# Kernel optimization log

Hardware: AMD Instinct MI355X
Metric: run time of the kernel (lower is better)

## Reference

```python
import jax, jax.numpy as jnp
import numpy as np

B, T, D_OBS, D_ACT, H = 1024, 1024, 32, 4, 64


def setup_inputs() -> dict:
    key = jax.random.key(0)
    ks = jax.random.split(key, 8)
    s = 0.1
    obs = jax.random.normal(ks[0], (B, T, D_OBS), dtype=jnp.float32)
    action = jax.random.normal(ks[1], (B, T, D_ACT), dtype=jnp.float32)
    # GRUCell params (torch layout): weight_ih [3H, Din], weight_hh [3H, H]
    W_ih = jax.random.normal(ks[2], (3 * H, D_OBS + D_ACT), dtype=jnp.float32) * s
    W_hh = jax.random.normal(ks[3], (3 * H, H), dtype=jnp.float32) * s
    b_ih = jax.random.normal(ks[4], (3 * H,), dtype=jnp.float32) * s
    b_hh = jax.random.normal(ks[5], (3 * H,), dtype=jnp.float32) * s
    # reward head: Linear(H, 1)
    W_r = jax.random.normal(ks[6], (1, H), dtype=jnp.float32) * s
    b_r = jax.random.normal(ks[7], (1,), dtype=jnp.float32) * s
    return {"obs": obs, "action": action, "W_ih": W_ih, "b_ih": b_ih,
            "W_hh": W_hh, "b_hh": b_hh, "W_r": W_r, "b_r": b_r}


def reference(obs, action, W_ih, b_ih, W_hh, b_hh, W_r, b_r):
    # x_t = cat(obs_t, action_t); GRUCell recurrence; reward = Linear(h_t)
    x = jnp.concatenate([obs, action], axis=-1)              # [B, T, Din]
    # Precompute input-to-hidden gates for all timesteps (batched GEMM)
    gi = jnp.einsum('btd,gd->btg', x, W_ih) + b_ih           # [B, T, 3H]
    gi_t = jnp.swapaxes(gi, 0, 1)                            # [T, B, 3H]

    def step(h, gi_step):
        gh = h @ W_hh.T + b_hh                               # [B, 3H]
        ghr, ghz, ghn = jnp.split(gh, 3, axis=-1)
        gir, giz, gin = jnp.split(gi_step, 3, axis=-1)
        r = jax.nn.sigmoid(gir + ghr)
        z = jax.nn.sigmoid(giz + ghz)
        n = jnp.tanh(gin + r * ghn)
        h_new = (1.0 - z) * n + z * h
        reward = h_new @ W_r.T + b_r                         # [B, 1]
        return h_new, reward

    h0 = jnp.zeros((obs.shape[0], H), dtype=obs.dtype)
    h_final, rewards = jax.lax.scan(step, h0, gi_t)          # rewards: [T, B, 1]
    return h_final, jnp.swapaxes(rewards, 0, 1)              # h: [B, H], reward: [B, T, 1]
```

## Files before the change

kernel.cpp:

```cpp
#include <hip/hip_runtime.h>


#define BB 1024
#define TT 1024
#define DOBS 32
#define DACT 4
#define HH 64

typedef __attribute__((ext_vector_type(8))) short short8;
typedef __attribute__((ext_vector_type(4))) float f32x4;

#define MFMA(A, B, C) __builtin_amdgcn_mfma_f32_16x16x32_bf16((A), (B), (C), 0, 0, 0)

static __device__ __forceinline__ unsigned short f2bf(float f) {
    unsigned u = __float_as_uint(f);
    u += 0x7fffu + ((u >> 16) & 1u);
    return (unsigned short)(u >> 16);
}
static __device__ __forceinline__ float frcp(float x) { return __builtin_amdgcn_rcpf(x); }
static __device__ __forceinline__ unsigned cvt_pk(float lo, float hi) {
    unsigned r;
    asm("v_cvt_pk_bf16_f32 %0, %1, %2" : "=v"(r) : "v"(lo), "v"(hi));
    return r;
}

#define L2E 1.442695040888963f

__global__ __launch_bounds__(256)
void pack_x(const float* __restrict__ obs, const float* __restrict__ act,
            unsigned short* __restrict__ xext)
{
    const size_t r = (size_t)blockIdx.x * 256 + threadIdx.x;
    const float* o = obs + r * DOBS;
    unsigned short* d = xext + r * 40;
    short8 v[5];
#pragma unroll
    for (int j = 0; j < 4; ++j) {
        float4 a = ((const float4*)o)[2 * j];
        float4 b = ((const float4*)o)[2 * j + 1];
        short8 t;
        t[0]=f2bf(a.x); t[1]=f2bf(a.y); t[2]=f2bf(a.z); t[3]=f2bf(a.w);
        t[4]=f2bf(b.x); t[5]=f2bf(b.y); t[6]=f2bf(b.z); t[7]=f2bf(b.w);
        v[j] = t;
    }
    {
        float4 a = *(const float4*)(act + r * DACT);
        short8 t;
        t[0]=f2bf(a.x); t[1]=f2bf(a.y); t[2]=f2bf(a.z); t[3]=f2bf(a.w);
        t[4]=(short)0x3f80; t[5]=0; t[6]=0; t[7]=0;
        v[4] = t;
    }
#pragma unroll
    for (int j = 0; j < 5; ++j) ((short8*)d)[j] = v[j];
}

#define LOADX(XO, XA, T)                                                       \
  {                                                                            \
    if (PACKED) {                                                              \
      XO = *(const short8*)(px + (size_t)(T) * 40 + 8 * q);                    \
      XA = (q == 0) ? *(const short8*)(px + (size_t)(T) * 40 + 32) : zero8;    \
    } else {                                                                   \
      const int tc_ = (T) < TT ? (T) : TT - 1;                                 \
      const float* op_ = po + (size_t)tc_ * DOBS + 8 * q;                      \
      float4 a_ = *(const float4*)op_, b_ = *(const float4*)(op_ + 4);         \
      short8 f_;                                                               \
      f_[0]=f2bf(a_.x); f_[1]=f2bf(a_.y); f_[2]=f2bf(a_.z); f_[3]=f2bf(a_.w);  \
      f_[4]=f2bf(b_.x); f_[5]=f2bf(b_.y); f_[6]=f2bf(b_.z); f_[7]=f2bf(b_.w);  \
      XO = f_;                                                                 \
      if (q == 0) {                                                            \
        float4 av_ = *(const float4*)(pa + (size_t)tc_ * DACT);                \
        short8 g_;                                                             \
        g_[0]=f2bf(av_.x); g_[1]=f2bf(av_.y); g_[2]=f2bf(av_.z);               \
        g_[3]=f2bf(av_.w); g_[4]=(short)0x3f80; g_[5]=0; g_[6]=0; g_[7]=0;     \
        XA = g_;                                                               \
      } else XA = zero8;                                                       \
    }                                                                          \
  }

#define HEAVY(PH, T, IT)                                                       \
  {                                                                            \
    __builtin_amdgcn_s_setprio(1);                                             \
    short8 Ah0 = *(const short8*)((const char*)hbuf[PH] + rdaddr0);            \
    short8 Ah1 = *(const short8*)((const char*)hbuf[PH] + rdaddr1);            \
    f32x4 hp = *(const f32x4*)((const char*)hf32[PH] + f32addr);               \
    f32x4 Cr  = MFMA(AH[0][1], Ah1, MFMA(AH[0][0], Ah0, cgr));                 \
    f32x4 Cz  = MFMA(AH[1][1], Ah1, MFMA(AH[1][0], Ah0, cgz));                 \
    f32x4 Cnh = MFMA(AH[2][1], Ah1, MFMA(AH[2][0], Ah0, bhn4));                \
    f32x4 Crw = zf;                                                            \
    const bool dorw_ = (w == ((IT) & 3));                                      \
    if (dorw_) Crw = MFMA(AR[1], Ah1, MFMA(AR[0], Ah0, zf));                   \
    _Pragma("unroll")                                                          \
    for (int reg = 0; reg < 4; ++reg) {                                        \
      float rr   = frcp(1.0f + __builtin_amdgcn_exp2f(Cr[reg]));               \
      float zz   = frcp(1.0f + __builtin_amdgcn_exp2f(Cz[reg]));               \
      float E    = __builtin_amdgcn_exp2f(__builtin_fmaf(rr, Cnh[reg], cgn[reg])); \
      float nn   = __builtin_fmaf(-2.0f, frcp(E + 1.0f), 1.0f);                \
      hold[reg]  = __builtin_fmaf(zz, hp[reg] - nn, nn);                       \
    }                                                                          \
    unsigned pk0 = cvt_pk(hold[0], hold[1]);                                   \
    unsigned pk1 = cvt_pk(hold[2], hold[3]);                                   \
    *(uint2*)((char*)hbuf[PH ^ 1] + wraddr) = make_uint2(pk0, pk1);            \
    *(f32x4*)((char*)hf32[PH ^ 1] + f32addr) = hold;                           \
    if (dorw_ && q == 0 && (T) > 0)                                            \
      rew[(size_t)(bid * 16 + c) * TT + (T) - 1] = Crw[0] + brr;               \
    asm volatile("s_waitcnt lgkmcnt(0)" ::: "memory");                         \
    __builtin_amdgcn_s_setprio(0);                                             \
  }

#define LIGHT(T2)                                                              \
  {                                                                            \
    cgr = MFMA(AX[0][1], xa, MFMA(AX[0][0], xo, zf));                          \
    cgz = MFMA(AX[1][1], xa, MFMA(AX[1][0], xo, zf));                          \
    cgn = MFMA(AX[2][1], xa, MFMA(AX[2][0], xo, zf));                          \
    LOADX(xo, xa, (T2) + 2)                                                    \
  }

template<bool PACKED>
__global__ __launch_bounds__(512, 1)
void gru_fused(const unsigned short* __restrict__ xext,
               const float* __restrict__ obs, const float* __restrict__ act,
               const float* __restrict__ W_ih, const float* __restrict__ b_ih,
               const float* __restrict__ W_hh, const float* __restrict__ b_hh,
               const float* __restrict__ W_r, const float* __restrict__ b_r,
               float* __restrict__ out)
{
    const int tid = threadIdx.x;
    const int set = tid >> 8;
    const int w = (tid >> 6) & 3;
    const int l = tid & 63, c = l & 15, q = l >> 4;
    const int bid = blockIdx.x;
    const int u0 = 16 * w + 4 * q;

    __shared__ __align__(16) unsigned short hbuf[2][16 * 64];
    __shared__ __align__(16) float          hf32[2][16 * 64];

    short8 AX[3][2], AH[3][2];
#pragma unroll
    for (int m = 0; m < 3; ++m) {
        const float sc = (m == 2) ? (2.0f * L2E) : (-L2E);
        const int j = w + 4 * m;
        const int g = 16 * j + c;
        {
            const float* wp = W_ih + (size_t)g * 36 + 8 * q;
            float4 a = *(const float4*)wp, b = *(const float4*)(wp + 4);
            short8 f;
            f[0]=f2bf(a.x*sc); f[1]=f2bf(a.y*sc); f[2]=f2bf(a.z*sc); f[3]=f2bf(a.w*sc);
            f[4]=f2bf(b.x*sc); f[5]=f2bf(b.y*sc); f[6]=f2bf(b.z*sc); f[7]=f2bf(b.w*sc);
            AX[m][0] = f;
        }
        {
            short8 f;
#pragma unroll
            for (int i = 0; i < 8; ++i) {
                int k = 32 + 8 * q + i;
                float v = 0.f;
                if (k < 36)       v = W_ih[(size_t)g * 36 + k];
                else if (k == 36) v = b_ih[g] + (g < 128 ? b_hh[g] : 0.f);
                f[i] = f2bf(v * sc);
            }
            AX[m][1] = f;
        }
#pragma unroll
        for (int kk = 0; kk < 2; ++kk) {
            const float* wp = W_hh + (size_t)g * HH + 32 * kk + 8 * q;
            float4 a = *(const float4*)wp, b = *(const float4*)(wp + 4);
            short8 f;
            f[0]=f2bf(a.x*sc); f[1]=f2bf(a.y*sc); f[2]=f2bf(a.z*sc); f[3]=f2bf(a.w*sc);
            f[4]=f2bf(b.x*sc); f[5]=f2bf(b.y*sc); f[6]=f2bf(b.z*sc); f[7]=f2bf(b.w*sc);
            AH[m][kk] = f;
        }
    }
    short8 AR[2];
#pragma unroll
    for (int kk = 0; kk < 2; ++kk) {
        short8 f;
#pragma unroll
        for (int i = 0; i < 8; ++i) {
            int k = 32 * kk + 8 * q + i;
            f[i] = (c == 0) ? (short)f2bf(W_r[k]) : (short)0;
        }
        AR[kk] = f;
    }

    f32x4 bhn4;
#pragma unroll
    for (int reg = 0; reg < 4; ++reg) bhn4[reg] = b_hh[128 + u0 + reg] * (2.0f * L2E);
    const float brr = b_r[0];

    const int swz = c & 7;
    const int wraddr  = c * 128 + ((((u0 >> 3)) ^ swz) << 4) + (u0 & 7) * 2;
    const int rdaddr0 = c * 128 + ((q ^ swz) << 4);
    const int rdaddr1 = c * 128 + (((4 + q) ^ swz) << 4);
    const int f32addr = c * 256 + (((4 * w + q) ^ swz) << 4);

    const size_t row = (size_t)(bid * 16 + c) * TT;
    const unsigned short* px = xext + row * 40;
    const float* po = obs + row * DOBS;
    const float* pa = act + row * DACT;

    const short8 zero8 = {0, 0, 0, 0, 0, 0, 0, 0};
    const f32x4 zf = {0.f, 0.f, 0.f, 0.f};

    ((uint2*)hbuf)[tid] = make_uint2(0u, 0u);
    ((f32x4*)hf32)[tid] = zf;
    short8 xo, xa;
    f32x4 cgr = zf, cgz = zf, cgn = zf;
    if (set == 0) {
        LOADX(xo, xa, 0)
        cgr = MFMA(AX[0][1], xa, MFMA(AX[0][0], xo, zf));
        cgz = MFMA(AX[1][1], xa, MFMA(AX[1][0], xo, zf));
        cgn = MFMA(AX[2][1], xa, MFMA(AX[2][0], xo, zf));
        LOADX(xo, xa, 2)
    } else {
        LOADX(xo, xa, 1)
    }
    f32x4 hold = zf;
    asm volatile("s_waitcnt lgkmcnt(0)" ::: "memory");
    __builtin_amdgcn_s_barrier();
    asm volatile("" ::: "memory");

    float* rew = out + (size_t)BB * HH;

#pragma unroll 1
    for (int it = 0; it < TT / 2; ++it) {
        const int Ta = 2 * it, Tb = 2 * it + 1;
        if (set == 0) { HEAVY(0, Ta, it) } else { LIGHT(Tb) }
        __builtin_amdgcn_s_barrier();
        asm volatile("" ::: "memory");
        if (set == 1) { HEAVY(1, Tb, it) } else { LIGHT(Ta + 2) }
        __builtin_amdgcn_s_barrier();
        asm volatile("" ::: "memory");
    }

    if (set == 1) {
        if (w == 3) {
            short8 Ah0 = *(const short8*)((const char*)hbuf[0] + rdaddr0);
            short8 Ah1 = *(const short8*)((const char*)hbuf[0] + rdaddr1);
            f32x4 Crw = MFMA(AR[0], Ah0, zf);
            Crw = MFMA(AR[1], Ah1, Crw);
            if (q == 0)
                rew[(size_t)(bid * 16 + c) * TT + TT - 1] = Crw[0] + brr;
        }
        *(float4*)(out + (size_t)(bid * 16 + c) * HH + u0) =
            make_float4(hold[0], hold[1], hold[2], hold[3]);
    }
}

extern "C" void kernel_launch(void* const* d_in, const int* in_sizes, int n_in,
                              void* d_out, int out_size, void* d_ws, size_t ws_size,
                              hipStream_t stream)
{
    const float* obs    = (const float*)d_in[0];
    const float* action = (const float*)d_in[1];
    const float* W_ih   = (const float*)d_in[2];
    const float* b_ih   = (const float*)d_in[3];
    const float* W_hh   = (const float*)d_in[4];
    const float* b_hh   = (const float*)d_in[5];
    const float* W_r    = (const float*)d_in[6];
    const float* b_r    = (const float*)d_in[7];
    float* out          = (float*)d_out;

    const size_t xext_bytes = ((size_t)BB * TT + 8) * 40 * sizeof(unsigned short);
    if (ws_size >= xext_bytes) {
        unsigned short* xext = (unsigned short*)d_ws;
        pack_x<<<dim3((BB * TT) / 256), dim3(256), 0, stream>>>(obs, action, xext);
        gru_fused<true><<<dim3(BB / 16), dim3(512), 0, stream>>>(
            xext, obs, action, W_ih, b_ih, W_hh, b_hh, W_r, b_r, out);
    } else {
        gru_fused<false><<<dim3(BB / 16), dim3(512), 0, stream>>>(
            nullptr, obs, action, W_ih, b_ih, W_hh, b_hh, W_r, b_r, out);
    }
}
```

Baseline: 398.7 us.

## Process two independent 16-row batch tiles per block to interleave recurrence chains

Each block now handles 32 batch rows as two independent 16-row tiles (X and Y), with separate LDS hidden-state buffers and duplicated MFMA/gate work. The grid shrinks from 64 to 32 blocks. The aim is to give the instruction scheduler two independent dependency chains to interleave, hiding MFMA and transcendental latency in the serial time loop. The trade-off is that only half as many CUs are used, on a GPU with far more CUs than blocks. The unpacked fallback path is replaced by a simple per-batch wave kernel.

```diff
diff --git a/kernel.cpp b/kernel.cpp
--- a/kernel.cpp
+++ b/kernel.cpp
@@ -54,71 +54,70 @@
     for (int j = 0; j < 5; ++j) ((short8*)d)[j] = v[j];
 }
 
-#define LOADX(XO, XA, T)                                                       \
+#define LOADX(PX, XO, XA, T)                                                   \
   {                                                                            \
-    if (PACKED) {                                                              \
-      XO = *(const short8*)(px + (size_t)(T) * 40 + 8 * q);                    \
-      XA = (q == 0) ? *(const short8*)(px + (size_t)(T) * 40 + 32) : zero8;    \
-    } else {                                                                   \
-      const int tc_ = (T) < TT ? (T) : TT - 1;                                 \
-      const float* op_ = po + (size_t)tc_ * DOBS + 8 * q;                      \
-      float4 a_ = *(const float4*)op_, b_ = *(const float4*)(op_ + 4);         \
-      short8 f_;                                                               \
-      f_[0]=f2bf(a_.x); f_[1]=f2bf(a_.y); f_[2]=f2bf(a_.z); f_[3]=f2bf(a_.w);  \
-      f_[4]=f2bf(b_.x); f_[5]=f2bf(b_.y); f_[6]=f2bf(b_.z); f_[7]=f2bf(b_.w);  \
-      XO = f_;                                                                 \
-      if (q == 0) {                                                            \
-        float4 av_ = *(const float4*)(pa + (size_t)tc_ * DACT);                \
-        short8 g_;                                                             \
-        g_[0]=f2bf(av_.x); g_[1]=f2bf(av_.y); g_[2]=f2bf(av_.z);               \
-        g_[3]=f2bf(av_.w); g_[4]=(short)0x3f80; g_[5]=0; g_[6]=0; g_[7]=0;     \
-        XA = g_;                                                               \
-      } else XA = zero8;                                                       \
+    XO = *(const short8*)((PX) + (size_t)(T) * 40 + 8 * q);                    \
+    XA = (q == 0) ? *(const short8*)((PX) + (size_t)(T) * 40 + 32) : zero8;    \
+  }
+
+#define GATES(CRF, CZF, CNHF, CNIF, HP, HOLD, HB, F32, PH)                     \
+    _Pragma("unroll")                                                          \
+    for (int reg = 0; reg < 4; ++reg) {                                        \
+      float rr   = frcp(1.0f + __builtin_amdgcn_exp2f(CRF[reg]));              \
+      float zz   = frcp(1.0f + __builtin_amdgcn_exp2f(CZF[reg]));              \
+      float E    = __builtin_amdgcn_exp2f(__builtin_fmaf(rr, CNHF[reg], CNIF[reg])); \
+      float nn   = __builtin_fmaf(-2.0f, frcp(E + 1.0f), 1.0f);                \
+      HOLD[reg]  = __builtin_fmaf(zz, HP[reg] - nn, nn);                       \
     }                                                                          \
-  }
+    *(uint2*)((char*)HB[PH ^ 1] + wraddr) =                                    \
+        make_uint2(cvt_pk(HOLD[0], HOLD[1]), cvt_pk(HOLD[2], HOLD[3]));        \
+    *(f32x4*)((char*)F32[PH ^ 1] + f32addr) = HOLD;
 
 #define HEAVY(PH, T, IT)                                                       \
   {                                                                            \
     __builtin_amdgcn_s_setprio(1);                                             \
-    short8 Ah0 = *(const short8*)((const char*)hbuf[PH] + rdaddr0);            \
-    short8 Ah1 = *(const short8*)((const char*)hbuf[PH] + rdaddr1);            \
-    f32x4 hp = *(const f32x4*)((const char*)hf32[PH] + f32addr);               \
-    f32x4 Cr  = MFMA(AH[0][1], Ah1, MFMA(AH[0][0], Ah0, cgr));                 \
-    f32x4 Cz  = MFMA(AH[1][1], Ah1, MFMA(AH[1][0], Ah0, cgz));                 \
-    f32x4 Cnh = MFMA(AH[2][1], Ah1, MFMA(AH[2][0], Ah0, bhn4));                \
-    f32x4 Crw = zf;                                                            \
+    short8 Ax0 = *(const short8*)((const char*)hbX[PH] + rdaddr0);             \
+    short8 Ax1 = *(const short8*)((const char*)hbX[PH] + rdaddr1);             \
+    short8 Ay0 = *(const short8*)((const char*)hbY[PH] + rdaddr0);             \
+    short8 Ay1 = *(const short8*)((const char*)hbY[PH] + rdaddr1);             \
+    f32x4 hpX = *(const f32x4*)((const char*)hfX[PH] + f32addr);               \
+    f32x4 hpY = *(const f32x4*)((const char*)hfY[PH] + f32addr);               \
+    f32x4 CrX  = MFMA(AH[0][1], Ax1, MFMA(AH[0][0], Ax0, cgrX));               \
+    f32x4 CrY  = MFMA(AH[0][1], Ay1, MFMA(AH[0][0], Ay0, cgrY));               \
+    f32x4 CzX  = MFMA(AH[1][1], Ax1, MFMA(AH[1][0], Ax0, cgzX));               \
+    f32x4 CzY  = MFMA(AH[1][1], Ay1, MFMA(AH[1][0], Ay0, cgzY));               \
+    f32x4 CnhX = MFMA(AH[2][1], Ax1, MFMA(AH[2][0], Ax0, bhn4));               \
+    f32x4 CnhY = MFMA(AH[2][1], Ay1, MFMA(AH[2][0], Ay0, bhn4));               \
+    f32x4 CrwX = zf, CrwY = zf;                                                \
     const bool dorw_ = (w == ((IT) & 3));                                      \
-    if (dorw_) Crw = MFMA(AR[1], Ah1, MFMA(AR[0], Ah0, zf));                   \
-    _Pragma("unroll")                                                          \
-    for (int reg = 0; reg < 4; ++reg) {                                        \
-      float rr   = frcp(1.0f + __builtin_amdgcn_exp2f(Cr[reg]));               \
-      float zz   = frcp(1.0f + __builtin_amdgcn_exp2f(Cz[reg]));               \
-      float E    = __builtin_amdgcn_exp2f(__builtin_fmaf(rr, Cnh[reg], cgn[reg])); \
-      float nn   = __builtin_fmaf(-2.0f, frcp(E + 1.0f), 1.0f);                \
-      hold[reg]  = __builtin_fmaf(zz, hp[reg] - nn, nn);                       \
+    if (dorw_) {                                                               \
+      CrwX = MFMA(AR[1], Ax1, MFMA(AR[0], Ax0, zf));                           \
+      CrwY = MFMA(AR[1], Ay1, MFMA(AR[0], Ay0, zf));                           \
     }                                                                          \
-    unsigned pk0 = cvt_pk(hold[0], hold[1]);                                   \
-    unsigned pk1 = cvt_pk(hold[2], hold[3]);                                   \
-    *(uint2*)((char*)hbuf[PH ^ 1] + wraddr) = make_uint2(pk0, pk1);            \
-    *(f32x4*)((char*)hf32[PH ^ 1] + f32addr) = hold;                           \
-    if (dorw_ && q == 0 && (T) > 0)                                            \
-      rew[(size_t)(bid * 16 + c) * TT + (T) - 1] = Crw[0] + brr;               \
+    GATES(CrX, CzX, CnhX, cgnX, hpX, holdX, hbX, hfX, PH)                      \
+    GATES(CrY, CzY, CnhY, cgnY, hpY, holdY, hbY, hfY, PH)                      \
+    if (dorw_ && q == 0 && (T) > 0) {                                          \
+      rew[(size_t)(bid * 32 + c) * TT + (T) - 1]      = CrwX[0] + brr;         \
+      rew[(size_t)(bid * 32 + 16 + c) * TT + (T) - 1] = CrwY[0] + brr;         \
+    }                                                                          \
     asm volatile("s_waitcnt lgkmcnt(0)" ::: "memory");                         \
     __builtin_amdgcn_s_setprio(0);                                             \
   }
 
 #define LIGHT(T2)                                                              \
   {                                                                            \
-    cgr = MFMA(AX[0][1], xa, MFMA(AX[0][0], xo, zf));                          \
-    cgz = MFMA(AX[1][1], xa, MFMA(AX[1][0], xo, zf));                          \
-    cgn = MFMA(AX[2][1], xa, MFMA(AX[2][0], xo, zf));                          \
-    LOADX(xo, xa, (T2) + 2)                                                    \
+    cgrX = MFMA(AX[0][1], xaX, MFMA(AX[0][0], xoX, zf));                       \
+    cgrY = MFMA(AX[0][1], xaY, MFMA(AX[0][0], xoY, zf));                       \
+    cgzX = MFMA(AX[1][1], xaX, MFMA(AX[1][0], xoX, zf));                       \
+    cgzY = MFMA(AX[1][1], xaY, MFMA(AX[1][0], xoY, zf));                       \
+    cgnX = MFMA(AX[2][1], xaX, MFMA(AX[2][0], xoX, zf));                       \
+    cgnY = MFMA(AX[2][1], xaY, MFMA(AX[2][0], xoY, zf));                       \
+    LOADX(pxX, xoX, xaX, (T2) + 2)                                             \
+    LOADX(pxY, xoY, xaY, (T2) + 2)                                             \
   }
 
-template<bool PACKED>
 __global__ __launch_bounds__(512, 1)
 void gru_fused(const unsigned short* __restrict__ xext,
-               const float* __restrict__ obs, const float* __restrict__ act,
                const float* __restrict__ W_ih, const float* __restrict__ b_ih,
                const float* __restrict__ W_hh, const float* __restrict__ b_hh,
                const float* __restrict__ W_r, const float* __restrict__ b_r,
@@ -131,8 +130,8 @@
     const int bid = blockIdx.x;
     const int u0 = 16 * w + 4 * q;
 
-    __shared__ __align__(16) unsigned short hbuf[2][16 * 64];
-    __shared__ __align__(16) float          hf32[2][16 * 64];
+    __shared__ __align__(16) unsigned short hbX[2][16 * 64], hbY[2][16 * 64];
+    __shared__ __align__(16) float          hfX[2][16 * 64], hfY[2][16 * 64];
 
     short8 AX[3][2], AH[3][2];
 #pragma unroll
@@ -193,28 +192,34 @@
     const int rdaddr1 = c * 128 + (((4 + q) ^ swz) << 4);
     const int f32addr = c * 256 + (((4 * w + q) ^ swz) << 4);
 
-    const size_t row = (size_t)(bid * 16 + c) * TT;
-    const unsigned short* px = xext + row * 40;
-    const float* po = obs + row * DOBS;
-    const float* pa = act + row * DACT;
+    const unsigned short* pxX = xext + ((size_t)(bid * 32 + c) * TT) * 40;
+    const unsigned short* pxY = xext + ((size_t)(bid * 32 + 16 + c) * TT) * 40;
 
     const short8 zero8 = {0, 0, 0, 0, 0, 0, 0, 0};
     const f32x4 zf = {0.f, 0.f, 0.f, 0.f};
 
-    ((uint2*)hbuf)[tid] = make_uint2(0u, 0u);
-    ((f32x4*)hf32)[tid] = zf;
-    short8 xo, xa;
-    f32x4 cgr = zf, cgz = zf, cgn = zf;
+    ((uint2*)hbX)[tid] = make_uint2(0u, 0u);
+    ((uint2*)hbY)[tid] = make_uint2(0u, 0u);
+    ((f32x4*)hfX)[tid] = zf;
+    ((f32x4*)hfY)[tid] = zf;
+    short8 xoX, xaX, xoY, xaY;
+    f32x4 cgrX = zf, cgzX = zf, cgnX = zf, cgrY = zf, cgzY = zf, cgnY = zf;
     if (set == 0) {
-        LOADX(xo, xa, 0)
-        cgr = MFMA(AX[0][1], xa, MFMA(AX[0][0], xo, zf));
-        cgz = MFMA(AX[1][1], xa, MFMA(AX[1][0], xo, zf));
-        cgn = MFMA(AX[2][1], xa, MFMA(AX[2][0], xo, zf));
-        LOADX(xo, xa, 2)
+        LOADX(pxX, xoX, xaX, 0)
+        LOADX(pxY, xoY, xaY, 0)
+        cgrX = MFMA(AX[0][1], xaX, MFMA(AX[0][0], xoX, zf));
+        cgrY = MFMA(AX[0][1], xaY, MFMA(AX[0][0], xoY, zf));
+        cgzX = MFMA(AX[1][1], xaX, MFMA(AX[1][0], xoX, zf));
+        cgzY = MFMA(AX[1][1], xaY, MFMA(AX[1][0], xoY, zf));
+        cgnX = MFMA(AX[2][1], xaX, MFMA(AX[2][0], xoX, zf));
+        cgnY = MFMA(AX[2][1], xaY, MFMA(AX[2][0], xoY, zf));
+        LOADX(pxX, xoX, xaX, 2)
+        LOADX(pxY, xoY, xaY, 2)
     } else {
-        LOADX(xo, xa, 1)
-    }
-    f32x4 hold = zf;
+        LOADX(pxX, xoX, xaX, 1)
+        LOADX(pxY, xoY, xaY, 1)
+    }
+    f32x4 holdX = zf, holdY = zf;
     asm volatile("s_waitcnt lgkmcnt(0)" ::: "memory");
     __builtin_amdgcn_s_barrier();
     asm volatile("" ::: "memory");
@@ -234,16 +239,74 @@
 
     if (set == 1) {
         if (w == 3) {
-            short8 Ah0 = *(const short8*)((const char*)hbuf[0] + rdaddr0);
-            short8 Ah1 = *(const short8*)((const char*)hbuf[0] + rdaddr1);
-            f32x4 Crw = MFMA(AR[0], Ah0, zf);
-            Crw = MFMA(AR[1], Ah1, Crw);
-            if (q == 0)
-                rew[(size_t)(bid * 16 + c) * TT + TT - 1] = Crw[0] + brr;
-        }
-        *(float4*)(out + (size_t)(bid * 16 + c) * HH + u0) =
-            make_float4(hold[0], hold[1], hold[2], hold[3]);
-    }
+            short8 Ax0 = *(const short8*)((const char*)hbX[0] + rdaddr0);
+            short8 Ax1 = *(const short8*)((const char*)hbX[0] + rdaddr1);
+            short8 Ay0 = *(const short8*)((const char*)hbY[0] + rdaddr0);
+            short8 Ay1 = *(const short8*)((const char*)hbY[0] + rdaddr1);
+            f32x4 CrwX = MFMA(AR[1], Ax1, MFMA(AR[0], Ax0, zf));
+            f32x4 CrwY = MFMA(AR[1], Ay1, MFMA(AR[0], Ay0, zf));
+            if (q == 0) {
+                rew[(size_t)(bid * 32 + c) * TT + TT - 1]      = CrwX[0] + brr;
+                rew[(size_t)(bid * 32 + 16 + c) * TT + TT - 1] = CrwY[0] + brr;
+            }
+        }
+        *(float4*)(out + (size_t)(bid * 32 + c) * HH + u0) =
+            make_float4(holdX[0], holdX[1], holdX[2], holdX[3]);
+        *(float4*)(out + (size_t)(bid * 32 + 16 + c) * HH + u0) =
+            make_float4(holdY[0], holdY[1], holdY[2], holdY[3]);
+    }
+}
+
+__global__ __launch_bounds__(64, 1)
+void gru_wave_fb(const float* __restrict__ obs, const float* __restrict__ action,
+                 const float* __restrict__ W_ih, const float* __restrict__ b_ih,
+                 const float* __restrict__ W_hh, const float* __restrict__ b_hh,
+                 const float* __restrict__ W_r, const float* __restrict__ b_r,
+                 float* __restrict__ out)
+{
+    const int b = blockIdx.x, j = threadIdx.x;
+    float wir[36], wiz[36], win[36];
+#pragma unroll
+    for (int d = 0; d < 36; ++d) {
+        wir[d] = W_ih[(size_t)(0 * HH + j) * 36 + d];
+        wiz[d] = W_ih[(size_t)(1 * HH + j) * 36 + d];
+        win[d] = W_ih[(size_t)(2 * HH + j) * 36 + d];
+    }
+    float whr[HH], whz[HH], whn[HH];
+#pragma unroll
+    for (int k = 0; k < HH; ++k) {
+        whr[k] = W_hh[(size_t)(0 * HH + j) * HH + k];
+        whz[k] = W_hh[(size_t)(1 * HH + j) * HH + k];
+        whn[k] = W_hh[(size_t)(2 * HH + j) * HH + k];
+    }
+    const float bir = b_ih[j], biz = b_ih[HH + j], bin = b_ih[2 * HH + j];
+    const float bhr = b_hh[j], bhz = b_hh[HH + j], bhn = b_hh[2 * HH + j];
+    const float wr = W_r[j], br = b_r[0];
+    float h = 0.f;
+    float* rew = out + (size_t)BB * HH;
+    for (int t = 0; t < TT; ++t) {
+        float x[36];
+#pragma unroll
+        for (int d = 0; d < DOBS; ++d) x[d] = obs[((size_t)b * TT + t) * DOBS + d];
+#pragma unroll
+        for (int d = 0; d < DACT; ++d) x[32 + d] = action[((size_t)b * TT + t) * DACT + d];
+        float gr = bir + bhr, gz = biz + bhz, gn = bin, an = bhn;
+#pragma unroll
+        for (int d = 0; d < 36; ++d) { gr += wir[d]*x[d]; gz += wiz[d]*x[d]; gn += win[d]*x[d]; }
+#pragma unroll
+        for (int k = 0; k < HH; ++k) {
+            float hk = __int_as_float(__builtin_amdgcn_readlane(__float_as_int(h), k));
+            gr += whr[k]*hk; gz += whz[k]*hk; an += whn[k]*hk;
+        }
+        float r = frcp(1.f + __expf(-gr)), z = frcp(1.f + __expf(-gz));
+        float n = 1.f - 2.f*frcp(__expf(2.f*(gn + r*an)) + 1.f);
+        h = n + z*(h - n);
+        float pr = h * wr;
+#pragma unroll
+        for (int m = 1; m < 64; m <<= 1) pr += __shfl_xor(pr, m, 64);
+        if (j == 0) rew[(size_t)b * TT + t] = pr + br;
+    }
+    out[(size_t)b * HH + j] = h;
 }
 
 extern "C" void kernel_launch(void* const* d_in, const int* in_sizes, int n_in,
@@ -264,10 +327,10 @@
     if (ws_size >= xext_bytes) {
         unsigned short* xext = (unsigned short*)d_ws;
         pack_x<<<dim3((BB * TT) / 256), dim3(256), 0, stream>>>(obs, action, xext);
-        gru_fused<true><<<dim3(BB / 16), dim3(512), 0, stream>>>(
-            xext, obs, action, W_ih, b_ih, W_hh, b_hh, W_r, b_r, out);
+        gru_fused<<<dim3(BB / 32), dim3(512), 0, stream>>>(
+            xext, W_ih, b_ih, W_hh, b_hh, W_r, b_r, out);
     } else {
-        gru_fused<false><<<dim3(BB / 16), dim3(512), 0, stream>>>(
-            nullptr, obs, action, W_ih, b_ih, W_hh, b_hh, W_r, b_r, out);
-    }
-}
+        gru_wave_fb<<<dim3(BB), dim3(64), 0, stream>>>(
+            obs, action, W_ih, b_ih, W_hh, b_hh, W_r, b_r, out);
+    }
+}
```

Result: slower. 626.8 us (+57.2%).

## Drop bf16 pack prekernel; load fp32 inputs directly with deeper prefetch

Applied to the files above, without the earlier changes.

Removes the separate pack_x kernel that converted obs/action to a bf16 workspace, so the recurrent kernel reads fp32 inputs straight from global memory. Raw loads are issued two steps ahead into registers and converted with packed cvt instructions just before use, hiding the extra load latency. This cuts a full extra pass over the input tensors and a kernel launch, at the cost of reading fp32 (larger) data inside the latency-critical loop and holding more registers.

```diff
diff --git a/kernel.cpp b/kernel.cpp
--- a/kernel.cpp
+++ b/kernel.cpp
@@ -26,55 +26,25 @@
 
 #define L2E 1.442695040888963f
 
-__global__ __launch_bounds__(256)
-void pack_x(const float* __restrict__ obs, const float* __restrict__ act,
-            unsigned short* __restrict__ xext)
-{
-    const size_t r = (size_t)blockIdx.x * 256 + threadIdx.x;
-    const float* o = obs + r * DOBS;
-    unsigned short* d = xext + r * 40;
-    short8 v[5];
-#pragma unroll
-    for (int j = 0; j < 4; ++j) {
-        float4 a = ((const float4*)o)[2 * j];
-        float4 b = ((const float4*)o)[2 * j + 1];
-        short8 t;
-        t[0]=f2bf(a.x); t[1]=f2bf(a.y); t[2]=f2bf(a.z); t[3]=f2bf(a.w);
-        t[4]=f2bf(b.x); t[5]=f2bf(b.y); t[6]=f2bf(b.z); t[7]=f2bf(b.w);
-        v[j] = t;
-    }
-    {
-        float4 a = *(const float4*)(act + r * DACT);
-        short8 t;
-        t[0]=f2bf(a.x); t[1]=f2bf(a.y); t[2]=f2bf(a.z); t[3]=f2bf(a.w);
-        t[4]=(short)0x3f80; t[5]=0; t[6]=0; t[7]=0;
-        v[4] = t;
-    }
-#pragma unroll
-    for (int j = 0; j < 5; ++j) ((short8*)d)[j] = v[j];
-}
-
-#define LOADX(XO, XA, T)                                                       \
-  {                                                                            \
-    if (PACKED) {                                                              \
-      XO = *(const short8*)(px + (size_t)(T) * 40 + 8 * q);                    \
-      XA = (q == 0) ? *(const short8*)(px + (size_t)(T) * 40 + 32) : zero8;    \
-    } else {                                                                   \
-      const int tc_ = (T) < TT ? (T) : TT - 1;                                 \
-      const float* op_ = po + (size_t)tc_ * DOBS + 8 * q;                      \
-      float4 a_ = *(const float4*)op_, b_ = *(const float4*)(op_ + 4);         \
-      short8 f_;                                                               \
-      f_[0]=f2bf(a_.x); f_[1]=f2bf(a_.y); f_[2]=f2bf(a_.z); f_[3]=f2bf(a_.w);  \
-      f_[4]=f2bf(b_.x); f_[5]=f2bf(b_.y); f_[6]=f2bf(b_.z); f_[7]=f2bf(b_.w);  \
-      XO = f_;                                                                 \
-      if (q == 0) {                                                            \
-        float4 av_ = *(const float4*)(pa + (size_t)tc_ * DACT);                \
-        short8 g_;                                                             \
-        g_[0]=f2bf(av_.x); g_[1]=f2bf(av_.y); g_[2]=f2bf(av_.z);               \
-        g_[3]=f2bf(av_.w); g_[4]=(short)0x3f80; g_[5]=0; g_[6]=0; g_[7]=0;     \
-        XA = g_;                                                               \
-      } else XA = zero8;                                                       \
-    }                                                                          \
+#define LOADR(T2)                                                              \
+  {                                                                            \
+    const int tc_ = (T2) < TT ? (T2) : TT - 1;                                 \
+    const float* op_ = po + (size_t)tc_ * DOBS + 8 * q;                        \
+    rawA = *(const float4*)op_;                                                \
+    rawB = *(const float4*)(op_ + 4);                                          \
+    if (q == 0) rawC = *(const float4*)(pa + (size_t)tc_ * DACT);              \
+  }
+
+#define CVTX(XO, XA)                                                           \
+  {                                                                            \
+    uint4 u_ = make_uint4(cvt_pk(rawA.x, rawA.y), cvt_pk(rawA.z, rawA.w),      \
+                          cvt_pk(rawB.x, rawB.y), cvt_pk(rawB.z, rawB.w));     \
+    XO = *(short8*)&u_;                                                        \
+    if (q == 0) {                                                              \
+      uint4 v_ = make_uint4(cvt_pk(rawC.x, rawC.y), cvt_pk(rawC.z, rawC.w),    \
+                            0x3f80u, 0u);                \
+      XA = *(short8*)&v_;                                                      \
+    } else XA = zero8;                                                         \
   }
 
 #define HEAVY(PH, T, IT)                                                       \
@@ -112,13 +82,12 @@
     cgr = MFMA(AX[0][1], xa, MFMA(AX[0][0], xo, zf));                          \
     cgz = MFMA(AX[1][1], xa, MFMA(AX[1][0], xo, zf));                          \
     cgn = MFMA(AX[2][1], xa, MFMA(AX[2][0], xo, zf));                          \
-    LOADX(xo, xa, (T2) + 2)                                                    \
-  }
-
-template<bool PACKED>
+    CVTX(xo, xa)                                                               \
+    LOADR((T2) + 4)                                                            \
+  }
+
 __global__ __launch_bounds__(512, 1)
-void gru_fused(const unsigned short* __restrict__ xext,
-               const float* __restrict__ obs, const float* __restrict__ act,
+void gru_fused(const float* __restrict__ obs, const float* __restrict__ act,
                const float* __restrict__ W_ih, const float* __restrict__ b_ih,
                const float* __restrict__ W_hh, const float* __restrict__ b_hh,
                const float* __restrict__ W_r, const float* __restrict__ b_r,
@@ -194,7 +163,6 @@
     const int f32addr = c * 256 + (((4 * w + q) ^ swz) << 4);
 
     const size_t row = (size_t)(bid * 16 + c) * TT;
-    const unsigned short* px = xext + row * 40;
     const float* po = obs + row * DOBS;
     const float* pa = act + row * DACT;
 
@@ -203,16 +171,19 @@
 
     ((uint2*)hbuf)[tid] = make_uint2(0u, 0u);
     ((f32x4*)hf32)[tid] = zf;
+    float4 rawA = make_float4(0,0,0,0), rawB = rawA, rawC = rawA;
     short8 xo, xa;
     f32x4 cgr = zf, cgz = zf, cgn = zf;
     if (set == 0) {
-        LOADX(xo, xa, 0)
+        LOADR(0) CVTX(xo, xa)
         cgr = MFMA(AX[0][1], xa, MFMA(AX[0][0], xo, zf));
         cgz = MFMA(AX[1][1], xa, MFMA(AX[1][0], xo, zf));
         cgn = MFMA(AX[2][1], xa, MFMA(AX[2][0], xo, zf));
-        LOADX(xo, xa, 2)
+        LOADR(2) CVTX(xo, xa)
+        LOADR(4)
     } else {
-        LOADX(xo, xa, 1)
+        LOADR(1) CVTX(xo, xa)
+        LOADR(3)
     }
     f32x4 hold = zf;
     asm volatile("s_waitcnt lgkmcnt(0)" ::: "memory");
@@ -260,14 +231,6 @@
     const float* b_r    = (const float*)d_in[7];
     float* out          = (float*)d_out;
 
-    const size_t xext_bytes = ((size_t)BB * TT + 8) * 40 * sizeof(unsigned short);
-    if (ws_size >= xext_bytes) {
-        unsigned short* xext = (unsigned short*)d_ws;
-        pack_x<<<dim3((BB * TT) / 256), dim3(256), 0, stream>>>(obs, action, xext);
-        gru_fused<true><<<dim3(BB / 16), dim3(512), 0, stream>>>(
-            xext, obs, action, W_ih, b_ih, W_hh, b_hh, W_r, b_r, out);
-    } else {
-        gru_fused<false><<<dim3(BB / 16), dim3(512), 0, stream>>>(
-            nullptr, obs, action, W_ih, b_ih, W_hh, b_hh, W_r, b_r, out);
-    }
-}
+    gru_fused<<<dim3(BB / 16), dim3(512), 0, stream>>>(
+        obs, action, W_ih, b_ih, W_hh, b_hh, W_r, b_r, out);
+}
```

Measured after the change: 427.4 us. 7.2% more time.
